# Kernel tuning notes

Measured on AMD Instinct MI355X. Metric: run time of the kernel, lower is better.

The kernel has to match this reference:

```python
import jax, jax.numpy as jnp
import numpy as np
from itertools import product

NC, AS = 2, 4          # nCodons, alphabet_size (hardcoded in the original __init__)
S, EM = 24, 6          # number of HMM states, emission alphabet size (alphabet_size + 2)
B_SZ, T = 512, 2048    # batch, sequence length

# ---- sparse structure of the transition matrix A (faithful to the TF index lists) ----

def _a_struct():
    off = 8 + 3 * NC
    idx = [(0, 0), (0, 1), (1, 2), (2, 3)]
    idx += [(3 + 3 * i, 4 + 3 * i) for i in range(NC)]
    idx += [(4 + 3 * i, 5 + 3 * i) for i in range(NC)]
    idx += [(5 + 3 * i, 6 + 3 * i) for i in range(NC)]
    idx += [(3 + 3 * i, off + 3 * i) for i in range(NC + 1)]   # inserts
    idx += [(3 + 3 * NC, 4 + 3 * NC)]
    idx += [(off + 3 * i, off + 1 + 3 * i) for i in range(NC + 1)]
    idx += [(off + 1 + 3 * i, off + 2 + 3 * i) for i in range(NC + 1)]
    idx += [(off + 2 + 3 * i, 4 + 3 * i) for i in range(NC + 1)]
    idx += [(off + 2 + 3 * i, off + 3 * i) for i in range(NC + 1)]
    i_del = [3 + 3 * i for i in range(NC) for _ in range(NC - i)]
    j_del = [4 + 3 * j for i in range(1, NC + 1) for j in range(i, NC + 1)]
    idx += list(zip(i_del, j_del))
    idx += [(4 + 3 * NC, 5 + 3 * NC), (5 + 3 * NC, 6 + 3 * NC), (6 + 3 * NC, 7 + 3 * NC),
            (7 + 3 * NC, 7 + 3 * NC), (7 + 3 * NC, off + 3 * (NC + 1)),
            (off + 3 * (NC + 1), off + 3 * (NC + 1))]
    pw = np.array([(j - i) // 3 for i, j in zip(i_del, j_del)], np.float32)
    return np.array(idx, np.int32), pw

A_IDX, DEL_PW = _a_struct()
A_MASK = np.zeros((S, S), bool)
A_MASK[A_IDX[:, 0], A_IDX[:, 1]] = True

# ---- sparse structure of the emission tensor B [S,6,6,6] ----

def _b_struct():
    idx, segs = [], []
    def W(n): segs.append(("w", n))
    def ONE(n): segs.append(("1", n))
    idx += [(0, i, j, l) for i in range(AS + 1) for j in range(max(AS, i + 1)) for l in range(AS)]; W((AS + 1) * AS ** 2 + 4)
    idx += [(1, i, j, 0) for i in range(AS + 1) for j in range(AS)]; W((AS + 1) * AS)
    idx += [(2, i, 0, 3) for i in range(AS)]; W(AS)
    idx += [(3, 0, 3, 2)]; ONE(1)
    idx += [(4, 3, 2, i) for i in range(AS)]; W(4)
    idx += [(5, 2, i, j) for i in range(AS) for j in range(AS)]; W(AS ** 2)
    idx += [(6 + i, j, k, l) for i in range(NC * 3 - 2) for j, k, l in product(range(AS), repeat=3)]; W((NC * 3 - 2) * AS ** 3)
    idx += [(4 + NC * 3, i, j, 3) for i, j in product(range(AS), repeat=2)]; W(AS ** 2)
    idx += [(5 + NC * 3, i, 3, 0) for i in range(AS)]; W(AS)
    idx += [(5 + NC * 3, i, 3, 2) for i in range(AS)]; W(AS)
    idx += [(6 + NC * 3, 3, 0, 0), (6 + NC * 3, 3, 0, 2), (6 + NC * 3, 3, 2, 0)]; ONE(3)
    idx += [(7 + NC * 3, i, j, l) for i, j, l in product(range(AS), repeat=3)]; W(AS ** 3)
    idx += [(8 + NC * 3 + l, i, j, m) for l in range(3 * (NC + 1)) for i, j, m in product(range(AS), repeat=3)]; W(AS ** 3 * 3 * (NC + 1))
    idx += [(8 + NC * 3 + (NC + 1) * 3, i, j, 5) for i, j in product(range(AS), repeat=2)]; W(AS ** 2)
    idx += [(8 + NC * 3 + (NC + 1) * 3, i, 5, 5) for i in range(AS)]; W(AS)
    idx += [(8 + NC * 3 + (NC + 1) * 3, 5, 5, 5)]; ONE(1)
    return np.array(idx, np.int32), segs

B_IDX, B_SEGS = _b_struct()
B_MASK = np.zeros((S, EM, EM, EM), bool)
B_MASK[B_IDX[:, 0], B_IDX[:, 1], B_IDX[:, 2], B_IDX[:, 3]] = True


def build_A(w):
    # values in the exact order the TF code concatenates them
    vals = jnp.concatenate([
        jnp.stack([1 - w[0], w[0]]),
        jnp.ones((2,), w.dtype),                       # (1,2),(2,3)
        w[1:1 + NC],                                   # codon entries
        jnp.ones((2 * NC,), w.dtype),                  # within-codon moves
        w[1 + NC:2 + 2 * NC],                          # insert entries
        (1 - w[1 + 2 * NC])[None],
        jnp.ones((2 * (NC + 1),), w.dtype),            # within-insert moves
        w[2 + 2 * NC:3 + 3 * NC],                      # insert -> codon
        1 - w[2 + 2 * NC:3 + 3 * NC],                  # insert self-loop
        1 - w[3 + 3 * NC] * w[3 + 3 * NC] ** jnp.asarray(DEL_PW, w.dtype),  # deletes
        jnp.ones((6,), w.dtype),                       # stop codon / terminal
    ])
    logits = jnp.zeros((S, S), w.dtype).at[A_IDX[:, 0], A_IDX[:, 1]].set(vals)
    mask = jnp.asarray(A_MASK)
    mx = jnp.max(jnp.where(mask, logits, -jnp.inf), axis=1, keepdims=True)
    e = jnp.where(mask, jnp.exp(logits - mx), 0.0)     # sparse softmax per row
    return e / e.sum(axis=1, keepdims=True)


def build_B(w):
    parts, k = [], 0
    for kind, n in B_SEGS:
        if kind == "w":
            parts.append(w[k:k + n]); k += n
        else:
            parts.append(jnp.ones((n,), w.dtype))
    vals = jnp.concatenate(parts)
    logits = jnp.zeros((S, EM, EM, EM), w.dtype).at[B_IDX[:, 0], B_IDX[:, 1], B_IDX[:, 2], B_IDX[:, 3]].set(vals)
    flat, mflat = logits.reshape(S, -1), jnp.asarray(B_MASK).reshape(S, -1)
    mx = jnp.max(jnp.where(mflat, flat, -jnp.inf), axis=1, keepdims=True)
    e = jnp.where(mflat, jnp.exp(flat - mx), 0.0)      # sparse softmax per state
    return (e / e.sum(axis=1, keepdims=True)).reshape(S, EM, EM, EM)


def setup_inputs() -> dict:
    key = jax.random.key(0)
    k1, k2, k3, k4 = jax.random.split(key, 4)
    return {
        "obs": jax.random.randint(k1, (B_SZ, T), 0, AS, dtype=jnp.int32),
        "transition_kernel": 0.05 * jax.random.normal(k2, (3 + 3 * NC + 1,), jnp.float32),
        "emission_kernel": 0.05 * jax.random.normal(k3, ((2 + NC * 3 + (NC + 1) * 3) * AS * 16,), jnp.float32),
        "init_kernel": 0.05 * jax.random.normal(k4, (S,), jnp.float32),
    }


def reference(obs, transition_kernel, emission_kernel, init_kernel):
    A = build_A(transition_kernel)                 # [S,S]
    Bm = build_B(emission_kernel)                  # [S,6,6,6]
    dt = transition_kernel.dtype
    x = jax.nn.one_hot(obs, EM, dtype=dt)          # [B,T,6]
    bsz = obs.shape[0]
    # sparse softmax of a single entry is exactly 1 at state 0
    i_vec = jnp.zeros((S,), dt).at[0].set(jax.nn.softmax(init_kernel[:1])[0])
    e4 = jnp.zeros((bsz, EM), dt).at[:, AS].set(1.0)   # "start" context one-hot (index 4)

    # t = 0: R = I^T, both previous inputs are the start context
    E0 = jnp.einsum("bl,sl->bs", x[:, 0], Bm[:, AS, AS, :])
    alpha0 = E0 * i_vec[None, :]
    Z0 = alpha0.sum(axis=1, keepdims=True)
    f0, ll0 = alpha0 / Z0, jnp.log(Z0)

    def step(carry, xt):
        f, ll, o2, o1 = carry
        R = f @ A                                   # [B,S]
        E = jnp.einsum("bj,bk,sjkl,bl->bs", o2, o1, Bm, xt)
        alpha = E * R
        Z = alpha.sum(axis=1, keepdims=True)
        f = alpha / Z                               # scaled forward
        return (f, ll + jnp.log(Z), o1, xt), f

    (_, loglik, _, _), fs = jax.lax.scan(step, (f0, ll0, e4, x[:, 0]), jnp.swapaxes(x[:, 1:], 0, 1))
    alphas = jnp.concatenate([f0[:, None], jnp.swapaxes(fs, 0, 1)], axis=1)  # [B,T,S]
    return alphas, loglik
```

## Files before the change

kernel.cpp:

```cpp
#include <hip/hip_runtime.h>

#define BATCH 512
#define TLEN  2048
#define NST   24
#define ESTR  28
#define NCTX  100
#define CBT   64
#define FPC   2
#define SLC   16

typedef float v2f __attribute__((ext_vector_type(2)));

__device__ __forceinline__ unsigned short f2bf(float x) {
  unsigned u = __float_as_uint(x);
  u += 0x7FFFu + ((u >> 16) & 1u);
  return (unsigned short)(u >> 16);
}

__device__ __forceinline__ float sload(const float* p) {
  return __uint_as_float(__builtin_amdgcn_readfirstlane(__float_as_uint(*p)));
}

__device__ __forceinline__ void at_update(const float* __restrict__ A,
                                          const float* __restrict__ f,
                                          float* __restrict__ R) {
  R[0]  = A[0]*f[0];
  R[1]  = A[1]*f[0];
  R[2]  = f[1];
  R[3]  = f[2];
  R[4]  = A[4]*f[3]  + A[24]*f[16];
  R[5]  = f[4];
  R[6]  = f[5];
  R[7]  = A[6]*f[3]  + A[10]*f[6] + A[28]*f[19];
  R[8]  = f[7];
  R[9]  = f[8];
  R[10] = A[7]*f[3]  + A[12]*f[6] + A[15]*f[9] + A[32]*f[22];
  R[11] = f[10];
  R[12] = f[11];
  R[13] = f[12] + A[20]*f[13];
  R[14] = A[5]*f[3]  + A[25]*f[16];
  R[15] = f[14];
  R[16] = f[15];
  R[17] = A[11]*f[6] + A[29]*f[19];
  R[18] = f[17];
  R[19] = f[18];
  R[20] = A[16]*f[9] + A[33]*f[22];
  R[21] = f[20];
  R[22] = f[21];
  R[23] = A[21]*f[13] + f[23];
}

__device__ __forceinline__ void at_update_pk(const float* __restrict__ A,
                                             const v2f* __restrict__ f,
                                             v2f* __restrict__ R) {
  R[0]  = A[0]*f[0];
  R[1]  = A[1]*f[0];
  R[2]  = f[1];
  R[3]  = f[2];
  R[4]  = A[4]*f[3]  + A[24]*f[16];
  R[5]  = f[4];
  R[6]  = f[5];
  R[7]  = A[6]*f[3]  + A[10]*f[6] + A[28]*f[19];
  R[8]  = f[7];
  R[9]  = f[8];
  R[10] = A[7]*f[3]  + A[12]*f[6] + A[15]*f[9] + A[32]*f[22];
  R[11] = f[10];
  R[12] = f[11];
  R[13] = f[12] + A[20]*f[13];
  R[14] = A[5]*f[3]  + A[25]*f[16];
  R[15] = f[14];
  R[16] = f[15];
  R[17] = A[11]*f[6] + A[29]*f[19];
  R[18] = f[17];
  R[19] = f[18];
  R[20] = A[16]*f[9] + A[33]*f[22];
  R[21] = f[20];
  R[22] = f[21];
  R[23] = A[21]*f[13] + f[23];
}

__device__ __forceinline__ float tree_sum24(const float* a) {
  float s0 = a[0]+a[1],   s1 = a[2]+a[3],   s2 = a[4]+a[5],   s3 = a[6]+a[7];
  float s4 = a[8]+a[9],   s5 = a[10]+a[11], s6 = a[12]+a[13], s7 = a[14]+a[15];
  float s8 = a[16]+a[17], s9 = a[18]+a[19], s10= a[20]+a[21], s11= a[22]+a[23];
  float u0 = s0+s1, u1 = s2+s3, u2 = s4+s5, u3 = s6+s7, u4 = s8+s9, u5 = s10+s11;
  return ((u0+u1) + (u2+u3)) + (u4+u5);
}

__device__ __forceinline__ void vec_step(const float* __restrict__ A,
                                         const float* __restrict__ ev,
                                         float* __restrict__ f) {
  float R[NST];
  at_update(A, f, R);
  float al[NST];
  #pragma unroll
  for (int s = 0; s < NST; ++s) al[s] = R[s] * ev[s];
  float z = tree_sum24(al);
  float zr = 1.0f / z;
  #pragma unroll
  for (int s = 0; s < NST; ++s) f[s] = al[s] * zr;
}

__device__ __forceinline__ void load_ev(const float4* __restrict__ etb, int ctx,
                                        float* __restrict__ ev) {
  const float4* ep = etb + ctx * 7;
  #pragma unroll
  for (int j = 0; j < 6; ++j) {
    float4 q = ep[j];
    ev[4*j] = q.x; ev[4*j+1] = q.y; ev[4*j+2] = q.z; ev[4*j+3] = q.w;
  }
}

__global__ __launch_bounds__(256) void k_prep(
    const int* __restrict__ obs,
    const float* __restrict__ wt, const float* __restrict__ we,
    float* __restrict__ etab, float* __restrict__ a35out,
    unsigned char* __restrict__ ctx8)
{
  if (blockIdx.x != 0) {
    int i = ((int)blockIdx.x - 1) * 256 + (int)threadIdx.x;
    int t = i & (TLEN - 1);
    int o0 = obs[i];
    int o1 = (t >= 1) ? obs[i-1] : 4;
    int o2 = (t >= 2) ? obs[i-2] : 4;
    ctx8[i] = (unsigned char)((o2*5 + o1)*4 + o0);
    return;
  }

  __shared__ float lg[NST * 216];
  __shared__ float pred[NST][8];
  __shared__ float rmx[NST];
  __shared__ float rrs[NST];
  int tid = threadIdx.x;
  for (int i = tid; i < NST * 216; i += 256) lg[i] = -1e30f;
  __syncthreads();

  for (int e = tid; e < 1073; e += 256) {
    int s, i, j, l, k = -1;
    if (e < 84)        { int ep=e; l=ep&3; int p=ep>>2; if (p<16){i=p>>2;j=p&3;} else {i=4;j=p-16;} s=0; k=ep; }
    else if (e < 104)  { int ep=e-84;  s=1;  i=ep>>2; j=ep&3; l=0; k=84+ep; }
    else if (e < 108)  { int ep=e-104; s=2;  i=ep;    j=0;    l=3; k=104+ep; }
    else if (e < 109)  { s=3; i=0; j=3; l=2; }
    else if (e < 113)  { int ep=e-109; s=4;  i=3; j=2; l=ep;  k=108+ep; }
    else if (e < 129)  { int ep=e-113; s=5;  i=2; j=ep>>2; l=ep&3; k=112+ep; }
    else if (e < 385)  { int ep=e-129; s=6+(ep>>6); int q=ep&63; i=q>>4; j=(q>>2)&3; l=q&3; k=128+ep; }
    else if (e < 401)  { int ep=e-385; s=10; i=ep>>2; j=ep&3; l=3; k=384+ep; }
    else if (e < 405)  { int ep=e-401; s=11; i=ep; j=3; l=0; k=400+ep; }
    else if (e < 409)  { int ep=e-405; s=11; i=ep; j=3; l=2; k=404+ep; }
    else if (e < 412)  { int ep=e-409; s=12; i=3; j=(ep==2)?2:0; l=(ep==1)?2:0; }
    else if (e < 476)  { int ep=e-412; s=13; i=ep>>4; j=(ep>>2)&3; l=ep&3; k=408+ep; }
    else if (e < 1052) { int ep=e-476; s=14+(ep>>6); int q=ep&63; i=q>>4; j=(q>>2)&3; l=q&3; k=472+ep; }
    else if (e < 1068) { int ep=e-1052; s=23; i=ep>>2; j=ep&3; l=5; k=1048+ep; }
    else if (e < 1072) { int ep=e-1068; s=23; i=ep; j=5; l=5; k=1064+ep; }
    else               { s=23; i=5; j=5; l=5; }
    float v = (k < 0) ? 1.0f : we[k];
    lg[s*216 + i*36 + j*6 + l] = v;
  }
  __syncthreads();

  if (tid < 192) {
    int s = tid >> 3, k = tid & 7;
    const float* base = lg + s*216 + k*27;
    float mx = base[0];
    for (int x = 1; x < 27; ++x) mx = fmaxf(mx, base[x]);
    pred[s][k] = mx;
  }
  __syncthreads();
  if (tid < NST) {
    float mx = pred[tid][0];
    #pragma unroll
    for (int k = 1; k < 8; ++k) mx = fmaxf(mx, pred[tid][k]);
    rmx[tid] = mx;
  }
  __syncthreads();
  if (tid < 192) {
    int s = tid >> 3, k = tid & 7;
    const float* base = lg + s*216 + k*27;
    float m = rmx[s];
    float sm = 0.f;
    for (int x = 0; x < 27; ++x) sm += __expf(base[x] - m);
    pred[s][k] = sm;
  }
  __syncthreads();
  if (tid < NST) {
    float sm = 0.f;
    #pragma unroll
    for (int k = 0; k < 8; ++k) sm += pred[tid][k];
    rrs[tid] = 1.0f / sm;
  }
  __syncthreads();

  if (tid < NCTX) {
    int c2 = tid / 20, c1 = (tid >> 2) % 5, c0 = tid & 3;
    int x = c2*36 + c1*6 + c0;
    float v[NST];
    float m = 1e-30f;
    for (int s = 0; s < NST; ++s) {
      v[s] = __expf(lg[s*216 + x] - rmx[s]) * rrs[s];
      m = fmaxf(m, v[s]);
    }
    float im = 1.0f / m;
    for (int s = 0; s < NST; ++s) etab[tid*ESTR + s] = v[s] * im;
    etab[tid*ESTR + 24] = __logf(m);
    etab[tid*ESTR + 25] = 0.f; etab[tid*ESTR + 26] = 0.f; etab[tid*ESTR + 27] = 0.f;
  }

  if (tid == 0) {
    float w[10];
    for (int q = 0; q < 10; ++q) w[q] = wt[q];
    float la[35];
    float d2 = 1.f - w[9]*w[9];
    float d3 = 1.f - w[9]*w[9]*w[9];
    la[0]=1.f-w[0]; la[1]=w[0];
    la[2]=1.f; la[3]=1.f;
    la[4]=w[1]; la[5]=w[3]; la[6]=d2; la[7]=d3;
    la[8]=1.f; la[9]=1.f;
    la[10]=w[2]; la[11]=w[4]; la[12]=d2;
    la[13]=1.f; la[14]=1.f;
    la[15]=1.f-w[5]; la[16]=w[5];
    la[17]=1.f; la[18]=1.f; la[19]=1.f;
    la[20]=1.f; la[21]=1.f;
    la[22]=1.f; la[23]=1.f;
    la[24]=w[6]; la[25]=1.f-w[6];
    la[26]=1.f; la[27]=1.f;
    la[28]=w[7]; la[29]=1.f-w[7];
    la[30]=1.f; la[31]=1.f;
    la[32]=w[8]; la[33]=1.f-w[8];
    la[34]=1.f;
    const int rs[25] = {0,2,3,4,8,9,10,13,14,15,17,18,19,20,22,23,24,26,27,28,30,31,32,34,35};
    for (int r = 0; r < 24; ++r) {
      float mx = -1e30f;
      for (int e = rs[r]; e < rs[r+1]; ++e) mx = fmaxf(mx, la[e]);
      float sm = 0.f;
      for (int e = rs[r]; e < rs[r+1]; ++e) sm += expf(la[e] - mx);
      float inv = 1.0f / sm;
      for (int e = rs[r]; e < rs[r+1]; ++e) a35out[e] = expf(la[e] - mx) * inv;
    }
  }
}

__global__ __launch_bounds__(256, 3) void k_phaseA(
    const unsigned char* __restrict__ ctx8,
    const float* __restrict__ etab,
    const float* __restrict__ a35,
    unsigned short* __restrict__ M,
    unsigned short* __restrict__ csumb,
    float* __restrict__ lsb)
{
  constexpr int L = TLEN / CBT;
  constexpr int GPA = 16;
  constexpr int WORDS = L / 4;
  __shared__ __align__(16) char smem[8 * NST * ESTR * 4];
  float* et = (float*)smem;
  for (int i = threadIdx.x; i < NCTX * ESTR; i += 256) et[i] = etab[i];
  float A[35];
  #pragma unroll
  for (int e = 0; e < 35; ++e) A[e] = sload(a35 + e);
  __syncthreads();

  int c   = (int)blockIdx.x / (BATCH / GPA);
  int bb  = (int)blockIdx.x % (BATCH / GPA);
  int grp = (int)threadIdx.x >> 4;
  int g   = (int)threadIdx.x & 15;
  int b   = bb * GPA + grp;
  bool act = g < 12;
  int col0 = g * 2;

  v2f m[NST];
  #pragma unroll
  for (int s = 0; s < NST; ++s) {
    m[s].x = (s == col0)     ? 1.0f : 0.0f;
    m[s].y = (s == col0 + 1) ? 1.0f : 0.0f;
  }

  const unsigned char* cb = ctx8 + (size_t)b * TLEN;
  const float4* etb = (const float4*)et;
  float ls = 0.0f;
  float lscx = 0.0f, lscy = 0.0f;
  const int t0 = c * L;

  int kk0 = 0;
  if (c == 0) {
    unsigned w = *(const unsigned*)cb;
    int ctx0 = (int)(w & 0xFFu);
    ls = __logf(et[ctx0*ESTR]) + et[ctx0*ESTR + 24];
    #pragma unroll
    for (int j = 1; j < 4; ++j) {
      int ctx = (int)((w >> (8*j)) & 0xFFu);
      float ev[NST];
      load_ev(etb, ctx, ev);
      ls += et[ctx*ESTR + 24];
      v2f R[NST];
      at_update_pk(A, m, R);
      #pragma unroll
      for (int s = 0; s < NST; ++s) m[s] = R[s] * ev[s];
    }
    kk0 = 1;
  }

  for (int kk = kk0; kk < WORDS; ++kk) {
    unsigned w = *(const unsigned*)(cb + t0 + kk*4);
    #pragma unroll
    for (int j = 0; j < 4; ++j) {
      int ctx = (int)((w >> (8*j)) & 0xFFu);
      float ev[NST];
      load_ev(etb, ctx, ev);
      ls += et[ctx*ESTR + 24];
      v2f R[NST];
      at_update_pk(A, m, R);
      #pragma unroll
      for (int s = 0; s < NST; ++s) m[s] = R[s] * ev[s];
    }
    if (kk == 3) {
      float cx = 0.f, cy = 0.f;
      #pragma unroll
      for (int s = 0; s < NST; ++s) { cx = fmaxf(cx, m[s].x); cy = fmaxf(cy, m[s].y); }
      float rx, ry;
      if (cx > 1e-35f) { lscx += __logf(cx); rx = 1.0f/cx; } else { lscx = -1e30f; rx = 0.f; }
      if (cy > 1e-35f) { lscy += __logf(cy); ry = 1.0f/cy; } else { lscy = -1e30f; ry = 0.f; }
      v2f rr; rr.x = rx; rr.y = ry;
      #pragma unroll
      for (int s = 0; s < NST; ++s) m[s] *= rr;
    }
  }

  {
    float cx = 0.f, cy = 0.f;
    #pragma unroll
    for (int s = 0; s < NST; ++s) { cx = fmaxf(cx, m[s].x); cy = fmaxf(cy, m[s].y); }
    float rx, ry;
    if (cx > 1e-35f) { lscx += __logf(cx); rx = 1.0f/cx; } else { lscx = -1e30f; rx = 0.f; }
    if (cy > 1e-35f) { lscy += __logf(cy); ry = 1.0f/cy; } else { lscy = -1e30f; ry = 0.f; }
    v2f rr; rr.x = rx; rr.y = ry;
    #pragma unroll
    for (int s = 0; s < NST; ++s) m[s] *= rr;
  }

  float tl = act ? fmaxf(lscx, lscy) : -1e30f;
  #pragma unroll
  for (int o = 1; o < 16; o <<= 1) tl = fmaxf(tl, __shfl_xor(tl, o, 16));
  float csm = tl;
  float facx = act ? __expf(lscx - csm) : 0.f;
  float facy = act ? __expf(lscy - csm) : 0.f;
  {
    v2f ff; ff.x = facx; ff.y = facy;
    #pragma unroll
    for (int s = 0; s < NST; ++s) m[s] *= ff;
  }

  if (act) {
    float sx = 0.f, sy = 0.f;
    #pragma unroll
    for (int s = 0; s < NST; ++s) { sx += m[s].x; sy += m[s].y; }
    ushort2 sv; sv.x = f2bf(sx); sv.y = f2bf(sy);
    *(ushort2*)(csumb + (size_t)(c*BATCH + b)*NST + col0) = sv;
  }

  __syncthreads();
  float (*tr)[NST][ESTR] = (float (*)[NST][ESTR])smem;
  #pragma unroll
  for (int pass = 0; pass < 2; ++pass) {
    int pg = grp - pass*8;
    bool in = (pg >= 0 && pg < 8);
    if (in && act) {
      #pragma unroll
      for (int s = 0; s < NST; ++s) {
        tr[pg][s][col0]   = m[s].x;
        tr[pg][s][col0+1] = m[s].y;
      }
    }
    __syncthreads();
    if (in && act) {
      #pragma unroll
      for (int rr2 = 0; rr2 < 2; ++rr2) {
        int row = col0 + rr2;
        const float4* rp = (const float4*)(&tr[pg][row][0]);
        float rowv[NST];
        #pragma unroll
        for (int j = 0; j < 6; ++j) {
          float4 q = rp[j];
          rowv[4*j] = q.x; rowv[4*j+1] = q.y; rowv[4*j+2] = q.z; rowv[4*j+3] = q.w;
        }
        unsigned pk[12];
        #pragma unroll
        for (int j = 0; j < 12; ++j)
          pk[j] = (unsigned)f2bf(rowv[2*j]) | ((unsigned)f2bf(rowv[2*j+1]) << 16);
        uint4* op = (uint4*)(M + ((size_t)(c*BATCH + b))*(NST*NST) + row*NST);
        op[0] = make_uint4(pk[0], pk[1], pk[2],  pk[3]);
        op[1] = make_uint4(pk[4], pk[5], pk[6],  pk[7]);
        op[2] = make_uint4(pk[8], pk[9], pk[10], pk[11]);
      }
    }
    __syncthreads();
  }
  if (g == 0) lsb[c*BATCH + b] = ls + csm;
}

__global__ __launch_bounds__(64) void k_phaseB(
    const unsigned short* __restrict__ M,
    const unsigned short* __restrict__ csumb,
    const float* __restrict__ lsb,
    float* __restrict__ vbc,
    float* __restrict__ alphas,
    float* __restrict__ llout)
{
  __shared__ __align__(16) float xfer[64];
  int lane = (int)threadIdx.x;
  int sub  = lane >> 5;
  int g    = lane & 31;
  bool act = g < NST;
  int gi   = act ? g : 0;
  int b    = (int)blockIdx.x * 2 + sub;

  float p[NST];
  #pragma unroll
  for (int j = 0; j < NST; ++j) p[j] = (j == 0) ? 1.0f : 0.0f;

  if (act) {
    vbc[((size_t)b*CBT + 0)*NST + g] = (g == 0) ? 1.0f : 0.0f;
    alphas[(size_t)b*TLEN*NST + g]   = (g == 0) ? 1.0f : 0.0f;
  }

  uint4 pfM[4][3];
  uint4 pfS[4][3];
  float pfL[4];
  #pragma unroll
  for (int i = 0; i < 4; ++i) {
    const uint4* mp = (const uint4*)(M + (((size_t)(i*BATCH + b))*NST + gi)*NST);
    pfM[i][0] = mp[0]; pfM[i][1] = mp[1]; pfM[i][2] = mp[2];
    const uint4* sp = (const uint4*)(csumb + (size_t)(i*BATCH + b)*NST);
    pfS[i][0] = sp[0]; pfS[i][1] = sp[1]; pfS[i][2] = sp[2];
    pfL[i] = lsb[i*BATCH + b];
  }

  float ll = 0.0f;
  for (int cc = 0; cc < CBT; cc += 4) {
    #pragma unroll
    for (int i = 0; i < 4; ++i) {
      int c = cc + i;
      float mr[NST];
      {
        unsigned uu[12] = {pfM[i][0].x,pfM[i][0].y,pfM[i][0].z,pfM[i][0].w,
                           pfM[i][1].x,pfM[i][1].y,pfM[i][1].z,pfM[i][1].w,
                           pfM[i][2].x,pfM[i][2].y,pfM[i][2].z,pfM[i][2].w};
        #pragma unroll
        for (int j = 0; j < 12; ++j) {
          mr[2*j]   = __uint_as_float(uu[j] << 16);
          mr[2*j+1] = __uint_as_float(uu[j] & 0xFFFF0000u);
        }
      }
      float sv[NST];
      {
        unsigned uu[12] = {pfS[i][0].x,pfS[i][0].y,pfS[i][0].z,pfS[i][0].w,
                           pfS[i][1].x,pfS[i][1].y,pfS[i][1].z,pfS[i][1].w,
                           pfS[i][2].x,pfS[i][2].y,pfS[i][2].z,pfS[i][2].w};
        #pragma unroll
        for (int j = 0; j < 12; ++j) {
          sv[2*j]   = __uint_as_float(uu[j] << 16);
          sv[2*j+1] = __uint_as_float(uu[j] & 0xFFFF0000u);
        }
      }
      float lsT = pfL[i];

      int cn = c + 4;
      if (cn < CBT) {
        const uint4* mp = (const uint4*)(M + (((size_t)(cn*BATCH + b))*NST + gi)*NST);
        pfM[i][0] = mp[0]; pfM[i][1] = mp[1]; pfM[i][2] = mp[2];
        const uint4* sp = (const uint4*)(csumb + (size_t)(cn*BATCH + b)*NST);
        pfS[i][0] = sp[0]; pfS[i][1] = sp[1]; pfS[i][2] = sp[2];
        pfL[i] = lsb[cn*BATCH + b];
      }

      float pr[NST], zz[NST];
      #pragma unroll
      for (int j = 0; j < NST; ++j) { pr[j] = mr[j] * p[j]; zz[j] = sv[j] * p[j]; }
      float nv = tree_sum24(pr);
      float z  = tree_sum24(zz);
      float zr = 1.0f / z;
      float fn = nv * zr;

      ll += __logf(z) + lsT;

      if (act && c + 1 < CBT) vbc[((size_t)b*CBT + c + 1)*NST + g] = fn;

      xfer[sub*32 + g] = fn;
      __syncthreads();
      {
        const float4* x4 = (const float4*)(&xfer[sub*32]);
        float4 q0 = x4[0], q1 = x4[1], q2 = x4[2],
               q3 = x4[3], q4 = x4[4], q5 = x4[5];
        p[0]=q0.x; p[1]=q0.y; p[2]=q0.z; p[3]=q0.w;
        p[4]=q1.x; p[5]=q1.y; p[6]=q1.z; p[7]=q1.w;
        p[8]=q2.x; p[9]=q2.y; p[10]=q2.z; p[11]=q2.w;
        p[12]=q3.x; p[13]=q3.y; p[14]=q3.z; p[15]=q3.w;
        p[16]=q4.x; p[17]=q4.y; p[18]=q4.z; p[19]=q4.w;
        p[20]=q5.x; p[21]=q5.y; p[22]=q5.z; p[23]=q5.w;
      }
      __syncthreads();
    }
  }
  if (g == 0) llout[b] = ll;
}

__global__ __launch_bounds__(256, 3) void k_phaseC(
    const unsigned char* __restrict__ ctx8,
    const float* __restrict__ etab,
    const float* __restrict__ a35,
    const float* __restrict__ vbc,
    float* __restrict__ alphas)
{
  constexpr int CL = TLEN / CBT;
  __shared__ __align__(16) float et[NCTX * ESTR];
  for (int i = threadIdx.x; i < NCTX * ESTR; i += 256) et[i] = etab[i];
  float A[35];
  #pragma unroll
  for (int e = 0; e < 35; ++e) A[e] = sload(a35 + e);
  __syncthreads();

  int wid = (int)blockIdx.x * 4 + ((int)threadIdx.x >> 6);
  int r   = wid / BATCH;
  int b   = wid % BATCH;
  int g   = (int)threadIdx.x & 63;

  float f[NST];
  {
    const float4* p = (const float4*)(vbc + ((size_t)b*CBT + g) * NST);
    #pragma unroll
    for (int j = 0; j < 6; ++j) {
      float4 q = p[j];
      f[4*j] = q.x; f[4*j+1] = q.y; f[4*j+2] = q.z; f[4*j+3] = q.w;
    }
  }

  const unsigned char* cb = ctx8 + (size_t)b * TLEN;
  const float4* etb = (const float4*)et;

  int t = g * CL;
  int n = r * SLC;
  for (int k = 0; k < n; ++k) {
    if (t != 0) {
      int ctx = cb[t];
      float ev[NST];
      load_ev(etb, ctx, ev);
      vec_step(A, ev, f);
    }
    ++t;
  }

  #pragma unroll
  for (int k = 0; k < SLC; ++k) {
    if (t != 0) {
      int ctx = cb[t];
      float ev[NST];
      load_ev(etb, ctx, ev);
      vec_step(A, ev, f);

      float4* o4 = (float4*)(alphas + ((size_t)b*TLEN + t) * NST);
      o4[0] = make_float4(f[0],  f[1],  f[2],  f[3]);
      o4[1] = make_float4(f[4],  f[5],  f[6],  f[7]);
      o4[2] = make_float4(f[8],  f[9],  f[10], f[11]);
      o4[3] = make_float4(f[12], f[13], f[14], f[15]);
      o4[4] = make_float4(f[16], f[17], f[18], f[19]);
      o4[5] = make_float4(f[20], f[21], f[22], f[23]);
    }
    ++t;
  }
}

extern "C" void kernel_launch(void* const* d_in, const int* in_sizes, int n_in,
                              void* d_out, int out_size, void* d_ws, size_t ws_size,
                              hipStream_t stream)
{
  (void)in_sizes; (void)n_in; (void)out_size; (void)ws_size;
  const int*   obs = (const int*)d_in[0];
  const float* wt  = (const float*)d_in[1];
  const float* we  = (const float*)d_in[2];

  float* out    = (float*)d_out;
  float* alphas = out;
  float* llout  = out + (size_t)BATCH * TLEN * NST;

  char* ws = (char*)d_ws;
  const size_t ETAB_OFF = 0;
  const size_t A_OFF    = 12 * 1024;
  const size_t CTX_OFF  = 16 * 1024;
  const size_t LS_OFF   = CTX_OFF + (size_t)BATCH * TLEN;
  const size_t CS_OFF   = LS_OFF + (size_t)CBT * BATCH * 4;
  const size_t VBC_OFF  = CS_OFF + (size_t)CBT * BATCH * NST * 2;
  const size_t M_OFF    = VBC_OFF + (size_t)BATCH * CBT * NST * 4;

  float* etab = (float*)(ws + ETAB_OFF);
  float* a35  = (float*)(ws + A_OFF);
  unsigned char* ctx8 = (unsigned char*)(ws + CTX_OFF);
  float* lsb  = (float*)(ws + LS_OFF);
  unsigned short* csumb = (unsigned short*)(ws + CS_OFF);
  float* vbc  = (float*)(ws + VBC_OFF);
  unsigned short* mbuf = (unsigned short*)(ws + M_OFF);

  k_prep<<<1 + (BATCH * TLEN) / 256, 256, 0, stream>>>(obs, wt, we, etab, a35, ctx8);
  k_phaseA<<<CBT * (BATCH / 16), 256, 0, stream>>>(ctx8, etab, a35, mbuf, csumb, lsb);
  k_phaseB<<<BATCH / 2, 64, 0, stream>>>(mbuf, csumb, lsb, vbc, alphas, llout);
  k_phaseC<<<(BATCH * FPC * 64) / 256, 256, 0, stream>>>(ctx8, etab, a35, vbc, alphas);
}
```

Measured before the change: 139.8 us.

## Stage phase-C alphas in LDS for coalesced writes with finer-grained chunk recompute

Phase C is reorganised so each block covers a 512-row window of one batch element. Each thread of 16 per chunk re-runs the forward recurrence from the chunk's start vector up to its own 2-step slice. The resulting normalized alphas go into a shared-memory buffer and are then written to global memory as contiguous float4 rows. This replaces widely strided per-thread stores with coalesced ones and raises parallelism, at the cost of much more redundant recurrence work, a large LDS allocation, and lower occupancy (launch bound 2).

```diff
diff --git a/kernel.cpp b/kernel.cpp
--- a/kernel.cpp
+++ b/kernel.cpp
@@ -6,8 +6,7 @@
 #define ESTR  28
 #define NCTX  100
 #define CBT   64
-#define FPC   2
-#define SLC   16
+#define WROWS 512
 
 typedef float v2f __attribute__((ext_vector_type(2)));
 
@@ -502,29 +501,33 @@
   if (g == 0) llout[b] = ll;
 }
 
-__global__ __launch_bounds__(256, 3) void k_phaseC(
+__global__ __launch_bounds__(256, 2) void k_phaseC(
     const unsigned char* __restrict__ ctx8,
     const float* __restrict__ etab,
     const float* __restrict__ a35,
     const float* __restrict__ vbc,
     float* __restrict__ alphas)
 {
-  constexpr int CL = TLEN / CBT;
+  constexpr int CL  = TLEN / CBT;
+  constexpr int CPW = WROWS / CL;
   __shared__ __align__(16) float et[NCTX * ESTR];
+  __shared__ __align__(16) float lbuf[WROWS * NST];
   for (int i = threadIdx.x; i < NCTX * ESTR; i += 256) et[i] = etab[i];
   float A[35];
   #pragma unroll
   for (int e = 0; e < 35; ++e) A[e] = sload(a35 + e);
   __syncthreads();
 
-  int wid = (int)blockIdx.x * 4 + ((int)threadIdx.x >> 6);
-  int r   = wid / BATCH;
-  int b   = wid % BATCH;
-  int g   = (int)threadIdx.x & 63;
+  int b   = (int)blockIdx.x >> 2;
+  int w   = (int)blockIdx.x & 3;
+  int tid = (int)threadIdx.x;
+  int cl  = tid >> 4;
+  int k   = tid & 15;
+  int cc  = w * CPW + cl;
 
   float f[NST];
   {
-    const float4* p = (const float4*)(vbc + ((size_t)b*CBT + g) * NST);
+    const float4* p = (const float4*)(vbc + ((size_t)b*CBT + cc) * NST);
     #pragma unroll
     for (int j = 0; j < 6; ++j) {
       float4 q = p[j];
@@ -535,9 +538,9 @@
   const unsigned char* cb = ctx8 + (size_t)b * TLEN;
   const float4* etb = (const float4*)et;
 
-  int t = g * CL;
-  int n = r * SLC;
-  for (int k = 0; k < n; ++k) {
+  int t = cc * CL;
+  int n = 2 * k;
+  for (int s = 0; s < n; ++s) {
     if (t != 0) {
       int ctx = cb[t];
       float ev[NST];
@@ -548,23 +551,29 @@
   }
 
   #pragma unroll
-  for (int k = 0; k < SLC; ++k) {
+  for (int j = 0; j < 2; ++j) {
     if (t != 0) {
       int ctx = cb[t];
       float ev[NST];
       load_ev(etb, ctx, ev);
       vec_step(A, ev, f);
-
-      float4* o4 = (float4*)(alphas + ((size_t)b*TLEN + t) * NST);
-      o4[0] = make_float4(f[0],  f[1],  f[2],  f[3]);
-      o4[1] = make_float4(f[4],  f[5],  f[6],  f[7]);
-      o4[2] = make_float4(f[8],  f[9],  f[10], f[11]);
-      o4[3] = make_float4(f[12], f[13], f[14], f[15]);
-      o4[4] = make_float4(f[16], f[17], f[18], f[19]);
-      o4[5] = make_float4(f[20], f[21], f[22], f[23]);
-    }
+    }
+    float4* d4 = (float4*)(&lbuf[(cl*CL + k*2 + j) * NST]);
+    d4[0] = make_float4(f[0],  f[1],  f[2],  f[3]);
+    d4[1] = make_float4(f[4],  f[5],  f[6],  f[7]);
+    d4[2] = make_float4(f[8],  f[9],  f[10], f[11]);
+    d4[3] = make_float4(f[12], f[13], f[14], f[15]);
+    d4[4] = make_float4(f[16], f[17], f[18], f[19]);
+    d4[5] = make_float4(f[20], f[21], f[22], f[23]);
     ++t;
   }
+  __syncthreads();
+
+  float4* gout = (float4*)(alphas + ((size_t)b*TLEN + (size_t)w*WROWS) * NST);
+  const float4* lsrc = (const float4*)lbuf;
+  #pragma unroll
+  for (int i = 0; i < (WROWS*NST)/(4*256); ++i)
+    gout[tid + 256*i] = lsrc[tid + 256*i];
 }
 
 extern "C" void kernel_launch(void* const* d_in, const int* in_sizes, int n_in,
@@ -600,5 +609,5 @@
   k_prep<<<1 + (BATCH * TLEN) / 256, 256, 0, stream>>>(obs, wt, we, etab, a35, ctx8);
   k_phaseA<<<CBT * (BATCH / 16), 256, 0, stream>>>(ctx8, etab, a35, mbuf, csumb, lsb);
   k_phaseB<<<BATCH / 2, 64, 0, stream>>>(mbuf, csumb, lsb, vbc, alphas, llout);
-  k_phaseC<<<(BATCH * FPC * 64) / 256, 256, 0, stream>>>(ctx8, etab, a35, vbc, alphas);
-}
+  k_phaseC<<<BATCH * (TLEN / WROWS), 256, 0, stream>>>(ctx8, etab, a35, vbc, alphas);
+}
```

Measured after the change: 173.3 us. +24.0%, slower.
